# Performance work log

Measured on AMD Instinct MI355X. Metric: run time of the kernel, lower is better.

Reference implementation:

```python
import jax, jax.numpy as jnp
import numpy as np

H = 128; W = 128; WH = 8; WW = 8; SH = 4; SW = 4
DIM = 512; HEADS = 16; HD = DIM // HEADS; HIDDEN = 2048
NH = H // WH; NW = W // WW; NWIN = NH * NW; WL = WH * WW
EPS = 1e-5
SCALE = HD ** -0.5


def _rel_pos_index():
    # Swin-style relative position index, static (WL, WL) int table
    coords = np.stack(np.meshgrid(np.arange(WH), np.arange(WW), indexing='ij')).reshape(2, -1)
    rel = (coords[:, :, None] - coords[:, None, :]).transpose(1, 2, 0)  # (WL, WL, 2)
    rel[:, :, 0] += WH - 1
    rel[:, :, 1] += WW - 1
    rel[:, :, 0] *= 2 * WW - 1
    return rel.sum(-1)  # (WL, WL), values in [0, (2WH-1)(2WW-1))


def _shift_attn_mask():
    # static shifted-window attention mask, (NWIN, WL, WL)
    m = np.zeros((H, W))
    cnt = 0
    for hs in (slice(0, -WH), slice(-WH, -SH), slice(-SH, None)):
        for ws in (slice(0, -WW), slice(-WW, -SW), slice(-SW, None)):
            m[hs, ws] = cnt
            cnt += 1
    mw = m.reshape(NH, WH, NW, WW).transpose(0, 2, 1, 3).reshape(NWIN, WL)
    am = mw[:, None, :] - mw[:, :, None]
    return np.where(am != 0, -100.0, 0.0).astype(np.float32)


_RPI = _rel_pos_index()
_MASK = _shift_attn_mask()


def _layernorm(x, w, b):
    mu = x.mean(-1, keepdims=True)
    var = ((x - mu) ** 2).mean(-1, keepdims=True)
    return (x - mu) / jnp.sqrt(var + EPS) * w + b


def _win_part(x):  # (H, W, D) -> (NWIN, WL, D)
    return x.reshape(NH, WH, NW, WW, DIM).transpose(0, 2, 1, 3, 4).reshape(NWIN, WL, DIM)


def _win_rev(w):  # (NWIN, WL, D) -> (H, W, D)
    return w.reshape(NH, NW, WH, WW, DIM).transpose(0, 2, 1, 3, 4).reshape(H, W, DIM)


def setup_inputs() -> dict:
    key = jax.random.key(0)
    ks = jax.random.split(key, 8)
    s = 0.02
    return {
        'x': jax.random.normal(ks[0], (H * W, DIM), dtype=jnp.float32),
        'ln1_w': jnp.ones((DIM,), jnp.float32),
        'ln1_b': jnp.zeros((DIM,), jnp.float32),
        'ln2_w': jnp.ones((DIM,), jnp.float32),
        'ln2_b': jnp.zeros((DIM,), jnp.float32),
        'qkv_w': jax.random.normal(ks[1], (3 * DIM, DIM), dtype=jnp.float32) * s,
        'qkv_b': jnp.zeros((3 * DIM,), jnp.float32),
        'proj_w': jax.random.normal(ks[2], (DIM, DIM), dtype=jnp.float32) * s,
        'proj_b': jnp.zeros((DIM,), jnp.float32),
        'rpb': jax.random.normal(ks[3], ((2 * WH - 1) * (2 * WW - 1), HEADS), dtype=jnp.float32) * s,
        'mlp_w1': jax.random.normal(ks[4], (HIDDEN, DIM), dtype=jnp.float32) * s,
        'mlp_b1': jnp.zeros((HIDDEN,), jnp.float32),
        'mlp_w2': jax.random.normal(ks[5], (DIM, HIDDEN), dtype=jnp.float32) * s,
        'mlp_b2': jnp.zeros((DIM,), jnp.float32),
    }


def reference(x, ln1_w, ln1_b, ln2_w, ln2_b, qkv_w, qkv_b, proj_w, proj_b, rpb,
              mlp_w1, mlp_b1, mlp_w2, mlp_b2):
    skip = x
    h = _layernorm(x, ln1_w, ln1_b).reshape(H, W, DIM)
    # cyclic shift + window partition
    h = jnp.roll(h, shift=(-SH, -SW), axis=(0, 1))
    xw = _win_part(h)  # (NWIN, WL, DIM)
    # windowed multi-head self-attention (equinox Linear: y = W @ x + b)
    qkv = jnp.einsum('nld,ed->nle', xw, qkv_w) + qkv_b
    q, k, v = [t.reshape(NWIN, WL, HEADS, HD).transpose(0, 2, 1, 3)
               for t in jnp.split(qkv, 3, axis=-1)]  # each (NWIN, HEADS, WL, HD)
    attn = jnp.einsum('nhqd,nhkd->nhqk', q * SCALE, k)
    bias = rpb[_RPI.reshape(-1)].reshape(WL, WL, HEADS).transpose(2, 0, 1)  # (HEADS, WL, WL)
    attn = attn + bias[None] + jnp.asarray(_MASK)[:, None]
    attn = jax.nn.softmax(attn, axis=-1)
    out = jnp.einsum('nhqk,nhkd->nhqd', attn, v).transpose(0, 2, 1, 3).reshape(NWIN, WL, DIM)
    out = jnp.einsum('nld,ed->nle', out, proj_w) + proj_b
    # window reverse + reverse cyclic shift
    h = jnp.roll(_win_rev(out), shift=(SH, SW), axis=(0, 1)).reshape(H * W, DIM)
    h = skip + h  # residual (drop_path is Identity at rate 0)
    # FFN branch (note: original code does x = x + drop_path(x), i.e. 2*mlp(norm2(.)))
    h = _layernorm(h, ln2_w, ln2_b)
    m = jax.nn.gelu(jnp.einsum('ld,ed->le', h, mlp_w1) + mlp_b1)
    m = jnp.einsum('le,de->ld', m, mlp_w2) + mlp_b2
    return m + m
```

## Files before the change

kernel.cpp:

```cpp
#include <hip/hip_runtime.h>
#include <hip/hip_bf16.h>
#include <stdint.h>

#define TOK   16384
#define DIMM  512
#define NHEAD 16
#define HDIM  32
#define HID   2048
#define NWIN  256
#define WLEN  64
#define EPSV  1e-5f
#define SCL   0.17677669529663687f

typedef __hip_bfloat16 bf16;
typedef __attribute__((ext_vector_type(8))) __bf16 bf16x8;
typedef __attribute__((ext_vector_type(4))) float f32x4;

__device__ __forceinline__ int remap_row(int r){
  int win = r >> 6, l = r & 63;
  int gh = ((win >> 4) << 3) + (l >> 3);
  int gw = ((win & 15) << 3) + (l & 7);
  int oh = (gh + 4) & 127, ow = (gw + 4) & 127;
  return (oh << 7) + ow;
}

__device__ __forceinline__ int region_of(int win, int l){
  int gh = ((win >> 4) << 3) + (l >> 3);
  int gw = ((win & 15) << 3) + (l & 7);
  int rh = (gh < 120) ? 0 : ((gh < 124) ? 1 : 2);
  int rw = (gw < 120) ? 0 : ((gw < 124) ? 1 : 2);
  return rh * 3 + rw;
}

__device__ __forceinline__ void gl_lds16(const bf16* g, bf16* l){
  __builtin_amdgcn_global_load_lds((const __attribute__((address_space(1))) void*)g,
                                   (__attribute__((address_space(3))) void*)l, 16, 0, 0);
}

__global__ __launch_bounds__(256) void convert_w(const float* __restrict__ a,
                                                 const float* __restrict__ b,
                                                 const float* __restrict__ c,
                                                 const float* __restrict__ d,
                                                 bf16* __restrict__ dst){
  int e = (blockIdx.x * 256 + threadIdx.x) * 4;
  float4 v;
  if (e < 786432)        v = *(const float4*)(a + e);
  else if (e < 1048576)  v = *(const float4*)(b + (e - 786432));
  else if (e < 2097152)  v = *(const float4*)(c + (e - 1048576));
  else                   v = *(const float4*)(d + (e - 2097152));
  union { bf16 h[4]; int2 q; } u;
  u.h[0] = __float2bfloat16(v.x); u.h[1] = __float2bfloat16(v.y);
  u.h[2] = __float2bfloat16(v.z); u.h[3] = __float2bfloat16(v.w);
  *(int2*)(dst + e) = u.q;
}

template<bool REMAP>
__global__ __launch_bounds__(256) void ln_kernel(const float* __restrict__ in,
    const float* __restrict__ w, const float* __restrict__ b, bf16* __restrict__ outp)
{
  const int wave = threadIdx.x >> 6, lane = threadIdx.x & 63;
  const int r = blockIdx.x * 4 + wave;
  const int src = REMAP ? remap_row(r) : r;
  const float4* row = (const float4*)(in + (size_t)src * DIMM);
  float4 v0 = row[lane*2], v1 = row[lane*2 + 1];
  float sm = v0.x+v0.y+v0.z+v0.w + v1.x+v1.y+v1.z+v1.w;
  float sq = v0.x*v0.x+v0.y*v0.y+v0.z*v0.z+v0.w*v0.w
           + v1.x*v1.x+v1.y*v1.y+v1.z*v1.z+v1.w*v1.w;
  #pragma unroll
  for (int off = 1; off < 64; off <<= 1){
    sm += __shfl_xor(sm, off);
    sq += __shfl_xor(sq, off);
  }
  const float mean = sm * (1.f/512.f);
  const float rstd = rsqrtf(sq*(1.f/512.f) - mean*mean + EPSV);
  const float4* wp = (const float4*)w; const float4* bp = (const float4*)b;
  float4 w0 = wp[lane*2], w1 = wp[lane*2+1], b0 = bp[lane*2], b1 = bp[lane*2+1];
  union { bf16 h[8]; int4 q; } u;
  u.h[0] = __float2bfloat16((v0.x-mean)*rstd*w0.x + b0.x);
  u.h[1] = __float2bfloat16((v0.y-mean)*rstd*w0.y + b0.y);
  u.h[2] = __float2bfloat16((v0.z-mean)*rstd*w0.z + b0.z);
  u.h[3] = __float2bfloat16((v0.w-mean)*rstd*w0.w + b0.w);
  u.h[4] = __float2bfloat16((v1.x-mean)*rstd*w1.x + b1.x);
  u.h[5] = __float2bfloat16((v1.y-mean)*rstd*w1.y + b1.y);
  u.h[6] = __float2bfloat16((v1.z-mean)*rstd*w1.z + b1.z);
  u.h[7] = __float2bfloat16((v1.w-mean)*rstd*w1.w + b1.w);
  *(int4*)(outp + (size_t)r*DIMM + lane*8) = u.q;
}

#define M_QKV  0
#define M_MLP1 2
#define M_PART 4

template<int KSTR>
__device__ __forceinline__ void stage_ht(const bf16* __restrict__ P,
                                         int grow0, bf16* lbase, int tid, int kt){
  const int r = tid >> 3;
  const int c = ((tid & 7) ^ (r & 7)) * 8;
  const bf16* g = P + (size_t)(grow0 + r) * KSTR + kt * 64 + c;
  bf16* l = lbase + r * 64 + (tid & 7) * 8;
  gl_lds16(g, l);
  gl_lds16(g + (size_t)64 * KSTR, l + 4096);
}

template<int MODE, int KEXT, int KSTR = KEXT>
__global__ __launch_bounds__(512, 1) void gemm8_bt(const bf16* __restrict__ A,
    const bf16* __restrict__ Wt, const float* __restrict__ bias,
    bf16* __restrict__ out_b, float* __restrict__ out_f, float* __restrict__ out_f2)
{
  constexpr int NT = KEXT / 64;
  extern __shared__ bf16 lds[];
  bf16* As = lds;
  bf16* Bs = lds + 32768;
  const int tid = threadIdx.x;
  const int ln = tid & 63, wv = tid >> 6;
  const int lrow = ln & 15, lgrp = ln >> 4;
  const int swz = lrow & 7;
  const int wm = wv >> 2, wn = wv & 3;
  const int m0 = blockIdx.x * 256, n0 = blockIdx.y * 256;

  if constexpr (MODE == M_PART){
    A  += blockIdx.z * 1024;
    Wt += blockIdx.z * 1024;
  }

  f32x4 acc[8][4] = {};
  bf16x8 aA0[4][2], aA1[4][2], bB0[2][2], bB1[2][2];

  #define LDA(DST, MH) { _Pragma("unroll") for (int mf = 0; mf < 4; mf++) \
    _Pragma("unroll") for (int ks = 0; ks < 2; ks++) \
      DST[mf][ks] = *(const bf16x8*)(As + s*16384 + (wm*128 + (MH)*64 + mf*16 + lrow)*64 + ((ks*4 + lgrp) ^ swz)*8); }
  #define LDB(DST, NH) { _Pragma("unroll") for (int nf = 0; nf < 2; nf++) \
    _Pragma("unroll") for (int ks = 0; ks < 2; ks++) \
      DST[nf][ks] = *(const bf16x8*)(Bs + s*16384 + (wn*64 + (NH)*32 + nf*16 + lrow)*64 + ((ks*4 + lgrp) ^ swz)*8); }
  #define QUAD(AR, BR, IM0, JN0) { _Pragma("unroll") for (int ks = 0; ks < 2; ks++) \
    _Pragma("unroll") for (int mf = 0; mf < 4; mf++) \
      _Pragma("unroll") for (int nf = 0; nf < 2; nf++) \
        acc[(IM0)+mf][(JN0)+nf] = __builtin_amdgcn_mfma_f32_16x16x32_bf16(AR[mf][ks], BR[nf][ks], acc[(IM0)+mf][(JN0)+nf], 0, 0, 0); }
  #define SBAR() { __builtin_amdgcn_sched_barrier(0); __builtin_amdgcn_s_barrier(); __builtin_amdgcn_sched_barrier(0); }
  #define LGKM(N) { asm volatile("s_waitcnt lgkmcnt(" #N ")" ::: "memory"); __builtin_amdgcn_sched_barrier(0); }

  stage_ht<KSTR>(A,  m0,       As,        tid, 0);
  stage_ht<KSTR>(Wt, n0,       Bs,        tid, 0);
  stage_ht<KSTR>(Wt, n0 + 128, Bs + 8192, tid, 0);
  stage_ht<KSTR>(A,  m0 + 128, As + 8192, tid, 0);
  asm volatile("s_waitcnt vmcnt(0)" ::: "memory");
  SBAR();
  stage_ht<KSTR>(Wt, n0,       Bs + 16384,        tid, 1);
  stage_ht<KSTR>(A,  m0,       As + 16384,        tid, 1);
  stage_ht<KSTR>(Wt, n0 + 128, Bs + 16384 + 8192, tid, 1);

  for (int t = 0; t < NT; ++t){
    const int s = t & 1;
    const int sx = s ^ 1;
    LDA(aA0, 0); LDB(bB0, 0);
    __builtin_amdgcn_sched_barrier(0);
    LDB(bB1, 1);
    if (t + 1 < NT) stage_ht<KSTR>(A, m0 + 128, As + sx*16384 + 8192, tid, t + 1);
    LGKM(4);
    __builtin_amdgcn_s_setprio(1); QUAD(aA0, bB0, 0, 0); __builtin_amdgcn_s_setprio(0);
    SBAR();
    LDA(aA1, 1);
    LGKM(8);
    __builtin_amdgcn_s_setprio(1); QUAD(aA0, bB1, 0, 2); __builtin_amdgcn_s_setprio(0);
    SBAR();
    if (t + 2 < NT) stage_ht<KSTR>(Wt, n0, Bs + s*16384, tid, t + 2);
    LGKM(0);
    __builtin_amdgcn_s_setprio(1); QUAD(aA1, bB1, 4, 2); __builtin_amdgcn_s_setprio(0);
    SBAR();
    if (t + 2 < NT){
      stage_ht<KSTR>(A,  m0,       As + s*16384,        tid, t + 2);
      stage_ht<KSTR>(Wt, n0 + 128, Bs + s*16384 + 8192, tid, t + 2);
    }
    __builtin_amdgcn_s_setprio(1); QUAD(aA1, bB0, 4, 0); __builtin_amdgcn_s_setprio(0);
    if (t == NT - 2)      { asm volatile("s_waitcnt vmcnt(0)" ::: "memory"); }
    else if (t < NT - 2)  { asm volatile("s_waitcnt vmcnt(6)" ::: "memory"); }
    SBAR();
  }
  #undef LDA
  #undef LDB
  #undef QUAD
  #undef SBAR
  #undef LGKM

  bf16* pdstb = nullptr;
  if constexpr (MODE == M_PART)
    pdstb = blockIdx.z ? (bf16*)out_f2 : (bf16*)out_f;
  #pragma unroll
  for (int im = 0; im < 8; im++){
    #pragma unroll
    for (int jn = 0; jn < 4; jn++){
      const int col = n0 + wn*64 + (jn >> 1)*32 + (jn & 1)*16 + lrow;
      const int row_b = m0 + wm*128 + (im >> 2)*64 + (im & 3)*16 + lgrp*4;
      const float bv = (MODE == M_PART) ? 0.f : bias[col];
      #pragma unroll
      for (int rr = 0; rr < 4; rr++){
        const int row = row_b + rr;
        float v = acc[im][jn][rr] + bv;
        if constexpr (MODE == M_QKV){
          const int t = col >> 9, rem = col & 511;
          const int head = rem >> 5, hd = rem & 31;
          const int win = row >> 6, l = row & 63;
          out_b[(size_t)t * (TOK*DIMM) + ((size_t)(win*NHEAD + head)*WLEN + l)*HDIM + hd]
              = __float2bfloat16(v);
        } else if constexpr (MODE == M_MLP1){
          const float u = 1.5957691216057308f * (v + 0.044715f*v*v*v);
          const float g = v * (1.0f / (1.0f + __expf(-u)));
          out_b[(size_t)row*HID + col] = __float2bfloat16(g);
        } else if constexpr (MODE == M_PART){
          pdstb[(size_t)row*DIMM + col] = __float2bfloat16(v);
        }
      }
    }
  }
}

__global__ __launch_bounds__(512, 1) void gemm_pl(const bf16* __restrict__ Ain,
    const bf16* __restrict__ Wt, const float* __restrict__ pb,
    const float* __restrict__ x, const float* __restrict__ w2,
    const float* __restrict__ b2, bf16* __restrict__ h2)
{
  extern __shared__ bf16 lds[];
  bf16* As = lds;
  bf16* Bs = lds + 4096;
  const int tid = threadIdx.x;
  const int ln = tid & 63, wv = tid >> 6;
  const int lrow = ln & 15, lgrp = ln >> 4;
  const int m0 = blockIdx.x * 64;

  f32x4 acc[4][4] = {};

  const int brow = tid >> 2;
  const int bchunk = ((tid & 3) ^ ((tid >> 3) & 3)) * 8;
  const int dst = brow * 32 + (tid & 3) * 8;

  #define STAGE(kt, sl) { \
    _Pragma("unroll") for (int i = 0; i < 4; i++) \
      gl_lds16(Wt + (size_t)(i*128 + brow)*DIMM + (kt)*32 + bchunk, Bs + (sl)*16384 + i*4096 + dst); \
    if (tid < 256) gl_lds16(Ain + (size_t)(m0 + brow)*DIMM + (kt)*32 + bchunk, As + (sl)*2048 + dst); \
  }

  const int rswz = (lgrp ^ ((lrow >> 1) & 3)) * 8;

  STAGE(0, 0);
  __syncthreads();
  for (int kt = 0; kt < 16; ++kt){
    const int s = kt & 1;
    if (kt + 1 < 16) STAGE(kt + 1, s ^ 1);
    bf16x8 a[4], b[4];
    #pragma unroll
    for (int mf = 0; mf < 4; mf++)
      a[mf] = *(const bf16x8*)(As + s*2048 + (mf*16 + lrow)*32 + rswz);
    #pragma unroll
    for (int nf = 0; nf < 4; nf++)
      b[nf] = *(const bf16x8*)(Bs + s*16384 + (wv*64 + nf*16 + lrow)*32 + rswz);
    #pragma unroll
    for (int mf = 0; mf < 4; mf++)
      #pragma unroll
      for (int nf = 0; nf < 4; nf++)
        acc[mf][nf] = __builtin_amdgcn_mfma_f32_16x16x32_bf16(a[mf], b[nf], acc[mf][nf], 0, 0, 0);
    __syncthreads();
  }
  #undef STAGE

  float* red = (float*)lds;
  #pragma unroll
  for (int mf = 0; mf < 4; mf++){
    #pragma unroll
    for (int rr = 0; rr < 4; rr++){
      const int r = mf*16 + lgrp*4 + rr;
      const int o = remap_row(m0 + r);
      float sm = 0.f, sq = 0.f;
      #pragma unroll
      for (int nf = 0; nf < 4; nf++){
        const int col = wv*64 + nf*16 + lrow;
        float v = acc[mf][nf][rr] + pb[col] + x[(size_t)o*DIMM + col];
        acc[mf][nf][rr] = v;
        sm += v; sq += v*v;
      }
      sm += __shfl_xor(sm, 1); sq += __shfl_xor(sq, 1);
      sm += __shfl_xor(sm, 2); sq += __shfl_xor(sq, 2);
      sm += __shfl_xor(sm, 4); sq += __shfl_xor(sq, 4);
      sm += __shfl_xor(sm, 8); sq += __shfl_xor(sq, 8);
      if (lrow == 0){ red[(wv*64 + r)*2] = sm; red[(wv*64 + r)*2 + 1] = sq; }
    }
  }
  __syncthreads();
  if (tid < 64){
    float sm = 0.f, sq = 0.f;
    #pragma unroll
    for (int w = 0; w < 8; w++){ sm += red[(w*64 + tid)*2]; sq += red[(w*64 + tid)*2 + 1]; }
    const float mean = sm * (1.f/512.f);
    const float var  = sq * (1.f/512.f) - mean*mean;
    red[tid*2]     = mean;
    red[tid*2 + 1] = rsqrtf(var + EPSV);
  }
  __syncthreads();
  #pragma unroll
  for (int mf = 0; mf < 4; mf++){
    #pragma unroll
    for (int rr = 0; rr < 4; rr++){
      const int r = mf*16 + lgrp*4 + rr;
      const int o = remap_row(m0 + r);
      const float mean = red[r*2], rstd = red[r*2 + 1];
      #pragma unroll
      for (int nf = 0; nf < 4; nf++){
        const int col = wv*64 + nf*16 + lrow;
        const float g = (acc[mf][nf][rr] - mean) * rstd * w2[col] + b2[col];
        h2[(size_t)o*DIMM + col] = __float2bfloat16(g);
      }
    }
  }
}

__global__ __launch_bounds__(256) void mlp2_reduce(const bf16* __restrict__ p0,
    const bf16* __restrict__ p1, float* __restrict__ dout, const float* __restrict__ bias){
  const size_t i = (size_t)(blockIdx.x * 256 + threadIdx.x) * 8;
  int4 a = *(const int4*)(p0 + i);
  int4 b = *(const int4*)(p1 + i);
  const int cb = (int)(i & 511);
  const float4 bv0 = *(const float4*)(bias + cb);
  const float4 bv1 = *(const float4*)(bias + cb + 4);
  const bf16* ah = (const bf16*)&a;
  const bf16* bh = (const bf16*)&b;
  float4 r0, r1;
  r0.x = 2.f*(__bfloat162float(ah[0]) + __bfloat162float(bh[0]) + bv0.x);
  r0.y = 2.f*(__bfloat162float(ah[1]) + __bfloat162float(bh[1]) + bv0.y);
  r0.z = 2.f*(__bfloat162float(ah[2]) + __bfloat162float(bh[2]) + bv0.z);
  r0.w = 2.f*(__bfloat162float(ah[3]) + __bfloat162float(bh[3]) + bv0.w);
  r1.x = 2.f*(__bfloat162float(ah[4]) + __bfloat162float(bh[4]) + bv1.x);
  r1.y = 2.f*(__bfloat162float(ah[5]) + __bfloat162float(bh[5]) + bv1.y);
  r1.z = 2.f*(__bfloat162float(ah[6]) + __bfloat162float(bh[6]) + bv1.z);
  r1.w = 2.f*(__bfloat162float(ah[7]) + __bfloat162float(bh[7]) + bv1.w);
  *(float4*)(dout + i)     = r0;
  *(float4*)(dout + i + 4) = r1;
}

__global__ __launch_bounds__(256) void attn_kernel(const bf16* __restrict__ qkv,
    const float* __restrict__ rpb, bf16* __restrict__ outp)
{
  __shared__ bf16 Pl[4][64][72];
  const int wave = threadIdx.x >> 6, lane = threadIdx.x & 63;
  const int lrow = lane & 15, lgrp = lane >> 4;
  const int wh = blockIdx.x * 4 + wave;
  const int win = wh >> 4, head = wh & 15;
  const bf16* qb = qkv + (size_t)wh * (WLEN*HDIM);
  const bf16* kb = qb + (size_t)TOK * DIMM;
  const bf16* vb = kb + (size_t)TOK * DIMM;

  bf16x8 aq[4], ak[4];
  #pragma unroll
  for (int i = 0; i < 4; i++){
    aq[i] = *(const bf16x8*)(qb + (i*16 + lrow)*HDIM + lgrp*8);
    ak[i] = *(const bf16x8*)(kb + (i*16 + lrow)*HDIM + lgrp*8);
  }
  f32x4 s[4][4] = {};
  #pragma unroll
  for (int i = 0; i < 4; i++)
    #pragma unroll
    for (int j = 0; j < 4; j++)
      s[i][j] = __builtin_amdgcn_mfma_f32_16x16x32_bf16(aq[i], ak[j], s[i][j], 0, 0, 0);

  #pragma unroll
  for (int i = 0; i < 4; i++){
    #pragma unroll
    for (int rr = 0; rr < 4; rr++){
      const int srow = i*16 + lgrp*4 + rr;
      const int rq = region_of(win, srow);
      float vals[4]; float mx = -1e30f;
      #pragma unroll
      for (int j = 0; j < 4; j++){
        const int scol = j*16 + lrow;
        const int idx = ((srow>>3) - (scol>>3) + 7)*15 + ((srow&7) - (scol&7) + 7);
        float v = s[i][j][rr]*SCL + rpb[idx*NHEAD + head];
        if (region_of(win, scol) != rq) v -= 100.f;
        vals[j] = v; mx = fmaxf(mx, v);
      }
      mx = fmaxf(mx, __shfl_xor(mx, 1));
      mx = fmaxf(mx, __shfl_xor(mx, 2));
      mx = fmaxf(mx, __shfl_xor(mx, 4));
      mx = fmaxf(mx, __shfl_xor(mx, 8));
      float sum = 0.f;
      #pragma unroll
      for (int j = 0; j < 4; j++){ vals[j] = __expf(vals[j] - mx); sum += vals[j]; }
      sum += __shfl_xor(sum, 1); sum += __shfl_xor(sum, 2);
      sum += __shfl_xor(sum, 4); sum += __shfl_xor(sum, 8);
      const float rs = 1.f / sum;
      #pragma unroll
      for (int j = 0; j < 4; j++)
        Pl[wave][srow][j*16 + lrow] = __float2bfloat16(vals[j] * rs);
    }
  }

  f32x4 o[4][2] = {};
  const __bf16* vraw = (const __bf16*)vb;
  #pragma unroll
  for (int st = 0; st < 2; st++){
    bf16x8 pa[4];
    #pragma unroll
    for (int i = 0; i < 4; i++)
      pa[i] = *(const bf16x8*)(&Pl[wave][i*16 + lrow][st*32 + lgrp*8]);
    bf16x8 bv[2];
    #pragma unroll
    for (int j = 0; j < 2; j++){
      #pragma unroll
      for (int jj = 0; jj < 8; jj++)
        bv[j][jj] = vraw[(size_t)(st*32 + lgrp*8 + jj)*HDIM + j*16 + lrow];
    }
    #pragma unroll
    for (int i = 0; i < 4; i++)
      #pragma unroll
      for (int j = 0; j < 2; j++)
        o[i][j] = __builtin_amdgcn_mfma_f32_16x16x32_bf16(pa[i], bv[j], o[i][j], 0, 0, 0);
  }
  bf16* orow = outp + (size_t)win * WLEN * DIMM + head * HDIM;
  #pragma unroll
  for (int i = 0; i < 4; i++)
    #pragma unroll
    for (int j = 0; j < 2; j++)
      #pragma unroll
      for (int rr = 0; rr < 4; rr++){
        const int l = i*16 + lgrp*4 + rr;
        orow[(size_t)l * DIMM + j*16 + lrow] = __float2bfloat16(o[i][j][rr]);
      }
}

extern "C" void kernel_launch(void* const* d_in, const int* in_sizes, int n_in,
                              void* d_out, int out_size, void* d_ws, size_t ws_size,
                              hipStream_t stream) {
  const float* x     = (const float*)d_in[0];
  const float* ln1w  = (const float*)d_in[1];
  const float* ln1b  = (const float*)d_in[2];
  const float* ln2w  = (const float*)d_in[3];
  const float* ln2b  = (const float*)d_in[4];
  const float* qkvw  = (const float*)d_in[5];
  const float* qkvbi = (const float*)d_in[6];
  const float* projw = (const float*)d_in[7];
  const float* projb = (const float*)d_in[8];
  const float* rpb   = (const float*)d_in[9];
  const float* m1w   = (const float*)d_in[10];
  const float* m1b   = (const float*)d_in[11];
  const float* m2w   = (const float*)d_in[12];
  const float* m2b   = (const float*)d_in[13];

  bf16* wqkv  = (bf16*)d_ws;
  bf16* wproj = wqkv + 786432;
  bf16* wm1   = wproj + 262144;
  bf16* wm2   = wm1 + 1048576;
  bf16* xw    = wm2 + 1048576;
  float* hbuf = (float*)(xw + 8388608);
  bf16* qkvb  = (bf16*)(hbuf + 8388608);
  bf16* attno = qkvb + 3*(size_t)8388608;
  bf16* m1buf = qkvb;
  bf16* h2    = xw;

  hipFuncSetAttribute((const void*)&gemm8_bt<M_QKV, 512>,
                      hipFuncAttributeMaxDynamicSharedMemorySize, 131072);
  hipFuncSetAttribute((const void*)&gemm8_bt<M_MLP1, 512>,
                      hipFuncAttributeMaxDynamicSharedMemorySize, 131072);
  hipFuncSetAttribute((const void*)&gemm8_bt<M_PART, 1024, 2048>,
                      hipFuncAttributeMaxDynamicSharedMemorySize, 131072);
  hipFuncSetAttribute((const void*)&gemm_pl,
                      hipFuncAttributeMaxDynamicSharedMemorySize, 73728);

  convert_w<<<3072, 256, 0, stream>>>(qkvw, projw, m1w, m2w, wqkv);
  ln_kernel<true><<<4096, 256, 0, stream>>>(x, ln1w, ln1b, xw);
  { dim3 g(TOK/256, 1536/256);
    gemm8_bt<M_QKV, 512><<<g, 512, 131072, stream>>>(xw, wqkv, qkvbi, qkvb, nullptr, nullptr); }
  attn_kernel<<<1024, 256, 0, stream>>>(qkvb, rpb, attno);
  gemm_pl<<<TOK/64, 512, 73728, stream>>>(attno, wproj, projb, x, ln2w, ln2b, h2);
  { dim3 g(TOK/256, 2048/256);
    gemm8_bt<M_MLP1, 512><<<g, 512, 131072, stream>>>(h2, wm1, m1b, m1buf, nullptr, nullptr); }
  { dim3 g(TOK/256, 512/256, 2);
    gemm8_bt<M_PART, 1024, 2048><<<g, 512, 131072, stream>>>(m1buf, wm2, m2b, nullptr,
                                                             (float*)hbuf, (float*)xw); }
  mlp2_reduce<<<8388608/8/256, 256, 0, stream>>>((const bf16*)hbuf, (const bf16*)xw,
                                                 (float*)d_out, m2b);
}
```

Before: 211.6 us.

## Replace 256x256 hand-pipelined GEMM with simpler 256x128 two-blocks-per-CU kernel

Swaps the 8-wave 256x256-tile GEMM, which used a hand-scheduled ping-pong pipeline with 128 KB of dynamic LDS, for a 4-wave kernel with 256x128 tiles. The new kernel uses a K-step of 32, static double-buffered LDS and a plain __syncthreads loop, with launch bounds that allow two blocks per CU. The aim is to rely on occupancy across blocks to hide latency instead of explicit intra-block scheduling. The cost is less operand reuse per tile, more global traffic for the A matrix, and no fine-grained overlap of MFMA with LDS loads.

```diff
diff --git a/kernel.cpp b/kernel.cpp
--- a/kernel.cpp
+++ b/kernel.cpp
@@ -91,111 +91,77 @@
 #define M_MLP1 2
 #define M_PART 4
 
-template<int KSTR>
-__device__ __forceinline__ void stage_ht(const bf16* __restrict__ P,
-                                         int grow0, bf16* lbase, int tid, int kt){
-  const int r = tid >> 3;
-  const int c = ((tid & 7) ^ (r & 7)) * 8;
-  const bf16* g = P + (size_t)(grow0 + r) * KSTR + kt * 64 + c;
-  bf16* l = lbase + r * 64 + (tid & 7) * 8;
-  gl_lds16(g, l);
-  gl_lds16(g + (size_t)64 * KSTR, l + 4096);
-}
-
 template<int MODE, int KEXT, int KSTR = KEXT>
-__global__ __launch_bounds__(512, 1) void gemm8_bt(const bf16* __restrict__ A,
+__global__ __launch_bounds__(256, 2) void gemm2b(const bf16* __restrict__ A,
     const bf16* __restrict__ Wt, const float* __restrict__ bias,
     bf16* __restrict__ out_b, float* __restrict__ out_f, float* __restrict__ out_f2)
 {
-  constexpr int NT = KEXT / 64;
-  extern __shared__ bf16 lds[];
-  bf16* As = lds;
-  bf16* Bs = lds + 32768;
+  constexpr int NT = KEXT / 32;
+  __shared__ bf16 As[2][256*32];
+  __shared__ bf16 Bs[2][128*32];
   const int tid = threadIdx.x;
   const int ln = tid & 63, wv = tid >> 6;
   const int lrow = ln & 15, lgrp = ln >> 4;
-  const int swz = lrow & 7;
-  const int wm = wv >> 2, wn = wv & 3;
-  const int m0 = blockIdx.x * 256, n0 = blockIdx.y * 256;
-
+  const int wm = wv >> 1, wn = wv & 1;
+  const int m0 = blockIdx.x * 256, n0 = blockIdx.y * 128;
+
+  const bf16* Ap = A;
+  const bf16* Bp = Wt;
   if constexpr (MODE == M_PART){
-    A  += blockIdx.z * 1024;
-    Wt += blockIdx.z * 1024;
+    Ap += blockIdx.z * 1024;
+    Bp += blockIdx.z * 1024;
   }
 
   f32x4 acc[8][4] = {};
-  bf16x8 aA0[4][2], aA1[4][2], bB0[2][2], bB1[2][2];
-
-  #define LDA(DST, MH) { _Pragma("unroll") for (int mf = 0; mf < 4; mf++) \
-    _Pragma("unroll") for (int ks = 0; ks < 2; ks++) \
-      DST[mf][ks] = *(const bf16x8*)(As + s*16384 + (wm*128 + (MH)*64 + mf*16 + lrow)*64 + ((ks*4 + lgrp) ^ swz)*8); }
-  #define LDB(DST, NH) { _Pragma("unroll") for (int nf = 0; nf < 2; nf++) \
-    _Pragma("unroll") for (int ks = 0; ks < 2; ks++) \
-      DST[nf][ks] = *(const bf16x8*)(Bs + s*16384 + (wn*64 + (NH)*32 + nf*16 + lrow)*64 + ((ks*4 + lgrp) ^ swz)*8); }
-  #define QUAD(AR, BR, IM0, JN0) { _Pragma("unroll") for (int ks = 0; ks < 2; ks++) \
-    _Pragma("unroll") for (int mf = 0; mf < 4; mf++) \
-      _Pragma("unroll") for (int nf = 0; nf < 2; nf++) \
-        acc[(IM0)+mf][(JN0)+nf] = __builtin_amdgcn_mfma_f32_16x16x32_bf16(AR[mf][ks], BR[nf][ks], acc[(IM0)+mf][(JN0)+nf], 0, 0, 0); }
-  #define SBAR() { __builtin_amdgcn_sched_barrier(0); __builtin_amdgcn_s_barrier(); __builtin_amdgcn_sched_barrier(0); }
-  #define LGKM(N) { asm volatile("s_waitcnt lgkmcnt(" #N ")" ::: "memory"); __builtin_amdgcn_sched_barrier(0); }
-
-  stage_ht<KSTR>(A,  m0,       As,        tid, 0);
-  stage_ht<KSTR>(Wt, n0,       Bs,        tid, 0);
-  stage_ht<KSTR>(Wt, n0 + 128, Bs + 8192, tid, 0);
-  stage_ht<KSTR>(A,  m0 + 128, As + 8192, tid, 0);
-  asm volatile("s_waitcnt vmcnt(0)" ::: "memory");
-  SBAR();
-  stage_ht<KSTR>(Wt, n0,       Bs + 16384,        tid, 1);
-  stage_ht<KSTR>(A,  m0,       As + 16384,        tid, 1);
-  stage_ht<KSTR>(Wt, n0 + 128, Bs + 16384 + 8192, tid, 1);
-
-  for (int t = 0; t < NT; ++t){
-    const int s = t & 1;
-    const int sx = s ^ 1;
-    LDA(aA0, 0); LDB(bB0, 0);
-    __builtin_amdgcn_sched_barrier(0);
-    LDB(bB1, 1);
-    if (t + 1 < NT) stage_ht<KSTR>(A, m0 + 128, As + sx*16384 + 8192, tid, t + 1);
-    LGKM(4);
-    __builtin_amdgcn_s_setprio(1); QUAD(aA0, bB0, 0, 0); __builtin_amdgcn_s_setprio(0);
-    SBAR();
-    LDA(aA1, 1);
-    LGKM(8);
-    __builtin_amdgcn_s_setprio(1); QUAD(aA0, bB1, 0, 2); __builtin_amdgcn_s_setprio(0);
-    SBAR();
-    if (t + 2 < NT) stage_ht<KSTR>(Wt, n0, Bs + s*16384, tid, t + 2);
-    LGKM(0);
-    __builtin_amdgcn_s_setprio(1); QUAD(aA1, bB1, 4, 2); __builtin_amdgcn_s_setprio(0);
-    SBAR();
-    if (t + 2 < NT){
-      stage_ht<KSTR>(A,  m0,       As + s*16384,        tid, t + 2);
-      stage_ht<KSTR>(Wt, n0 + 128, Bs + s*16384 + 8192, tid, t + 2);
-    }
-    __builtin_amdgcn_s_setprio(1); QUAD(aA1, bB0, 4, 0); __builtin_amdgcn_s_setprio(0);
-    if (t == NT - 2)      { asm volatile("s_waitcnt vmcnt(0)" ::: "memory"); }
-    else if (t < NT - 2)  { asm volatile("s_waitcnt vmcnt(6)" ::: "memory"); }
-    SBAR();
-  }
-  #undef LDA
-  #undef LDB
-  #undef QUAD
-  #undef SBAR
-  #undef LGKM
+
+  const int r0 = tid >> 2, c4 = tid & 3;
+  const int sc = (c4 ^ ((r0 >> 1) & 3)) * 8;
+  const int dst0 = r0 * 32 + c4 * 8;
+
+  #define STAGE(kt, sl) { \
+    _Pragma("unroll") for (int i = 0; i < 4; i++) \
+      gl_lds16(Ap + (size_t)(m0 + i*64 + r0) * KSTR + (kt)*32 + sc, As[sl] + i*2048 + dst0); \
+    _Pragma("unroll") for (int i = 0; i < 2; i++) \
+      gl_lds16(Bp + (size_t)(n0 + i*64 + r0) * KSTR + (kt)*32 + sc, Bs[sl] + i*2048 + dst0); \
+  }
+
+  const int pc = (lgrp ^ ((lrow >> 1) & 3)) * 8;
+
+  STAGE(0, 0);
+  __syncthreads();
+  for (int kt = 0; kt < NT; ++kt){
+    const int s = kt & 1;
+    if (kt + 1 < NT) STAGE(kt + 1, s ^ 1);
+    bf16x8 a[8], b[4];
+    #pragma unroll
+    for (int mf = 0; mf < 8; mf++)
+      a[mf] = *(const bf16x8*)(&As[s][(wm*128 + mf*16 + lrow)*32 + pc]);
+    #pragma unroll
+    for (int nf = 0; nf < 4; nf++)
+      b[nf] = *(const bf16x8*)(&Bs[s][(wn*64 + nf*16 + lrow)*32 + pc]);
+    #pragma unroll
+    for (int mf = 0; mf < 8; mf++)
+      #pragma unroll
+      for (int nf = 0; nf < 4; nf++)
+        acc[mf][nf] = __builtin_amdgcn_mfma_f32_16x16x32_bf16(a[mf], b[nf], acc[mf][nf], 0, 0, 0);
+    __syncthreads();
+  }
+  #undef STAGE
 
   bf16* pdstb = nullptr;
   if constexpr (MODE == M_PART)
     pdstb = blockIdx.z ? (bf16*)out_f2 : (bf16*)out_f;
   #pragma unroll
-  for (int im = 0; im < 8; im++){
-    #pragma unroll
-    for (int jn = 0; jn < 4; jn++){
-      const int col = n0 + wn*64 + (jn >> 1)*32 + (jn & 1)*16 + lrow;
-      const int row_b = m0 + wm*128 + (im >> 2)*64 + (im & 3)*16 + lgrp*4;
+  for (int mf = 0; mf < 8; mf++){
+    #pragma unroll
+    for (int nf = 0; nf < 4; nf++){
+      const int col = n0 + wn*64 + nf*16 + lrow;
+      const int row_b = m0 + wm*128 + mf*16 + lgrp*4;
       const float bv = (MODE == M_PART) ? 0.f : bias[col];
       #pragma unroll
       for (int rr = 0; rr < 4; rr++){
         const int row = row_b + rr;
-        float v = acc[im][jn][rr] + bv;
+        float v = acc[mf][nf][rr] + bv;
         if constexpr (MODE == M_QKV){
           const int t = col >> 9, rem = col & 511;
           const int head = rem >> 5, hd = rem & 31;
@@ -453,26 +419,20 @@
   bf16* m1buf = qkvb;
   bf16* h2    = xw;
 
-  hipFuncSetAttribute((const void*)&gemm8_bt<M_QKV, 512>,
-                      hipFuncAttributeMaxDynamicSharedMemorySize, 131072);
-  hipFuncSetAttribute((const void*)&gemm8_bt<M_MLP1, 512>,
-                      hipFuncAttributeMaxDynamicSharedMemorySize, 131072);
-  hipFuncSetAttribute((const void*)&gemm8_bt<M_PART, 1024, 2048>,
-                      hipFuncAttributeMaxDynamicSharedMemorySize, 131072);
   hipFuncSetAttribute((const void*)&gemm_pl,
                       hipFuncAttributeMaxDynamicSharedMemorySize, 73728);
 
   convert_w<<<3072, 256, 0, stream>>>(qkvw, projw, m1w, m2w, wqkv);
   ln_kernel<true><<<4096, 256, 0, stream>>>(x, ln1w, ln1b, xw);
-  { dim3 g(TOK/256, 1536/256);
-    gemm8_bt<M_QKV, 512><<<g, 512, 131072, stream>>>(xw, wqkv, qkvbi, qkvb, nullptr, nullptr); }
+  { dim3 g(TOK/256, 1536/128);
+    gemm2b<M_QKV, 512><<<g, 256, 0, stream>>>(xw, wqkv, qkvbi, qkvb, nullptr, nullptr); }
   attn_kernel<<<1024, 256, 0, stream>>>(qkvb, rpb, attno);
   gemm_pl<<<TOK/64, 512, 73728, stream>>>(attno, wproj, projb, x, ln2w, ln2b, h2);
-  { dim3 g(TOK/256, 2048/256);
-    gemm8_bt<M_MLP1, 512><<<g, 512, 131072, stream>>>(h2, wm1, m1b, m1buf, nullptr, nullptr); }
-  { dim3 g(TOK/256, 512/256, 2);
-    gemm8_bt<M_PART, 1024, 2048><<<g, 512, 131072, stream>>>(m1buf, wm2, m2b, nullptr,
-                                                             (float*)hbuf, (float*)xw); }
+  { dim3 g(TOK/256, 2048/128);
+    gemm2b<M_MLP1, 512><<<g, 256, 0, stream>>>(h2, wm1, m1b, m1buf, nullptr, nullptr); }
+  { dim3 g(TOK/256, 512/128, 2);
+    gemm2b<M_PART, 1024, 2048><<<g, 256, 0, stream>>>(m1buf, wm2, m2b, nullptr,
+                                                      (float*)hbuf, (float*)xw); }
   mlp2_reduce<<<8388608/8/256, 256, 0, stream>>>((const bf16*)hbuf, (const bf16*)xw,
                                                  (float*)d_out, m2b);
 }
```

Result: slower. 242.2 us (+14.5%).
